# Kernel tuning notes

Measured on AMD Instinct MI355X. Metric: run time of the kernel, lower is better.

## Reference

```python
import jax, jax.numpy as jnp
import numpy as np

GRID_SIZE = 5
SPLINE_ORDER = 3
GRID_RANGE = (-0.2, 0.2)
N_TOK, IN_CH, OUT_CH = 8192, 1024, 1024
K_COEF = GRID_SIZE + SPLINE_ORDER  # 8 basis functions per feature


def _make_grid():
    lo, hi = GRID_RANGE
    h = (hi - lo) / GRID_SIZE
    # 12 knots, extended by spline_order on both sides
    return (jnp.arange(-SPLINE_ORDER, GRID_SIZE + SPLINE_ORDER + 1, dtype=jnp.float32) * h + lo)


def _b_splines(x, grid):
    # x: [N, in] -> bases: [N, in, K_COEF] via Cox-de Boor recursion
    xe = x[..., None]                      # [N, in, 1]
    G = grid.shape[0]                      # 12
    bases = ((xe >= grid[:-1]) & (xe < grid[1:])).astype(x.dtype)  # [N, in, G-1]
    for k in range(1, SPLINE_ORDER + 1):
        left = (xe - grid[: G - k - 1]) / (grid[k : G - 1] - grid[: G - k - 1]) * bases[..., :-1]
        right = (grid[k + 1 :] - xe) / (grid[k + 1 :] - grid[1 : G - k]) * bases[..., 1:]
        bases = left + right
    return bases                            # [N, in, 8]


def _kan_layer(x, base_w, spline_w, grid):
    # base_activation = Identity
    base_out = x @ base_w.T                               # [N, out]
    bases = _b_splines(x, grid)                           # [N, in, K]
    spline_out = jnp.einsum('nik,oik->no', bases, spline_w)
    return base_out + spline_out


def setup_inputs() -> dict:
    key = jax.random.key(0)
    k1, k2, k3, k4, k5 = jax.random.split(key, 5)
    lo, hi = GRID_RANGE
    x = jax.random.uniform(k1, (N_TOK, IN_CH), dtype=jnp.float32, minval=lo, maxval=hi)
    s = 0.1 / np.sqrt(IN_CH)
    return {
        'x': x,
        'base_w1': jax.random.normal(k2, (OUT_CH, IN_CH), dtype=jnp.float32) * s,
        'spline_w1': jax.random.normal(k3, (OUT_CH, IN_CH, K_COEF), dtype=jnp.float32) * s,
        'base_w2': jax.random.normal(k4, (OUT_CH, OUT_CH), dtype=jnp.float32) * s,
        'spline_w2': jax.random.normal(k5, (OUT_CH, OUT_CH, K_COEF), dtype=jnp.float32) * s,
    }


def reference(x, base_w1, spline_w1, base_w2, spline_w2):
    grid = _make_grid()
    x1 = _kan_layer(x, base_w1, spline_w1, grid)
    x2 = _kan_layer(x1, base_w2, spline_w2, grid)
    return x2
```

## Files before the change

kernel.cpp:

```cpp
#include <hip/hip_runtime.h>
#include <hip/hip_bf16.h>

typedef __attribute__((ext_vector_type(8))) short bf16x8;
typedef __attribute__((ext_vector_type(4))) float f32x4;

#define KCAT 9216
#define NTOK 8192
#define CH   1024
#define KHALF 4608
#define BK   64
#define NT   (KHALF / BK)

__device__ __forceinline__ unsigned short f2bf(float f) {
    union { float f; unsigned int u; } v; v.f = f;
    unsigned int r = v.u + 0x7fffu + ((v.u >> 16) & 1u);
    return (unsigned short)(r >> 16);
}

__device__ __forceinline__ void load16_to_lds(const void* gp, void* lp) {
    __builtin_amdgcn_global_load_lds(
        (__attribute__((address_space(1))) void*)(void*)gp,
        (__attribute__((address_space(3))) void*)lp,
        16, 0, 0);
}

__device__ __forceinline__ void bases8(float x, unsigned short* out8) {
    const float h = 0.08f;
    float t[12];
#pragma unroll
    for (int j = 0; j < 12; ++j) t[j] = -0.2f + h * (float)(j - 3);
    const float r1 = 1.0f / h, r2 = 1.0f / (2.0f * h), r3 = 1.0f / (3.0f * h);
    float b[11];
#pragma unroll
    for (int j = 0; j < 11; ++j) b[j] = (x >= t[j] && x < t[j + 1]) ? 1.0f : 0.0f;
#pragma unroll
    for (int j = 0; j < 10; ++j) b[j] = (x - t[j]) * r1 * b[j] + (t[j + 2] - x) * r1 * b[j + 1];
#pragma unroll
    for (int j = 0; j < 9; ++j)  b[j] = (x - t[j]) * r2 * b[j] + (t[j + 3] - x) * r2 * b[j + 1];
#pragma unroll
    for (int j = 0; j < 8; ++j)  b[j] = (x - t[j]) * r3 * b[j] + (t[j + 4] - x) * r3 * b[j + 1];
#pragma unroll
    for (int j = 0; j < 8; ++j) out8[j] = f2bf(b[j]);
}

__global__ __launch_bounds__(256) void conv_w(const float* __restrict__ BW,
                                              const float* __restrict__ SW,
                                              unsigned short* __restrict__ W) {
    int o = blockIdx.x;
    const float* bw = BW + (size_t)o * 1024;
    const float* sw = SW + (size_t)o * 8192;
    unsigned short* w = W + (size_t)o * KCAT;
    for (int c = threadIdx.x * 4; c < KCAT; c += 256 * 4) {
        const float* src = (c < 1024) ? (bw + c) : (sw + (c - 1024));
        float4 v = *(const float4*)src;
        unsigned short u[4] = { f2bf(v.x), f2bf(v.y), f2bf(v.z), f2bf(v.w) };
        *(unsigned long long*)(w + c) = *(unsigned long long*)u;
    }
}

__global__ __launch_bounds__(256) void kan_basis_x(const float* __restrict__ X,
                                                   unsigned short* __restrict__ A,
                                                   int total) {
    for (int idx = blockIdx.x * 256 + threadIdx.x; idx < total; idx += gridDim.x * 256) {
        int n = idx >> 10, i = idx & 1023;
        float x = X[idx];
        size_t rowbase = (size_t)n * KCAT;
        A[rowbase + i] = f2bf(x);
        unsigned short out8[8];
        bases8(x, out8);
        *(bf16x8*)(A + rowbase + 1024 + (size_t)i * 8) = *(bf16x8*)out8;
    }
}

__global__ __launch_bounds__(256) void kan_basis_sum(const float* __restrict__ C0,
                                                     const float* __restrict__ C1,
                                                     unsigned short* __restrict__ A,
                                                     int total) {
    for (int idx = blockIdx.x * 256 + threadIdx.x; idx < total; idx += gridDim.x * 256) {
        int n = idx >> 10, i = idx & 1023;
        float x = C0[idx] + C1[idx];
        size_t rowbase = (size_t)n * KCAT;
        A[rowbase + i] = f2bf(x);
        unsigned short out8[8];
        bases8(x, out8);
        *(bf16x8*)(A + rowbase + 1024 + (size_t)i * 8) = *(bf16x8*)out8;
    }
}

__global__ __launch_bounds__(256) void add_out(const float* __restrict__ C0,
                                               const float* __restrict__ C1,
                                               float* __restrict__ out, int total4) {
    for (int i = blockIdx.x * 256 + threadIdx.x; i < total4; i += gridDim.x * 256) {
        float4 a = ((const float4*)C0)[i];
        float4 b = ((const float4*)C1)[i];
        float4 r = { a.x + b.x, a.y + b.y, a.z + b.z, a.w + b.w };
        ((float4*)out)[i] = r;
    }
}

__global__ __launch_bounds__(512, 2) void gemm256_splitk(const unsigned short* __restrict__ A,
                                                         const unsigned short* __restrict__ B,
                                                         float* __restrict__ C0,
                                                         float* __restrict__ C1) {
    __shared__ unsigned short As[2 * 256 * 64];
    __shared__ unsigned short Bs[2 * 256 * 64];
    const int tid  = threadIdx.x;
    const int lane = tid & 63;
    const int wid  = tid >> 6;
    const int wr = wid >> 2, wc = wid & 3;
    const int ln = lane & 15, q = lane >> 4;

    const int bid = blockIdx.x;
    const int xcd = bid & 7, i = bid >> 3;
    const int kz = xcd & 1, chm = xcd >> 1;
    const int bm = chm * 8 + (i & 7);
    const int bn = i >> 3;

    const unsigned short* Ab = A + (size_t)(bm * 256) * KCAT + (size_t)kz * KHALF;
    const unsigned short* Bb = B + (size_t)(bn * 256) * KCAT + (size_t)kz * KHALF;
    float* C = (kz == 0) ? C0 : C1;

    f32x4 acc[8][4] = {};

    auto stage = [&](int t, int buf, int part) {
        int chunk = part * 512 + tid;
        int r    = chunk >> 3;
        int slot = (chunk & 7) ^ (r & 7);
        size_t goff = (size_t)r * (KCAT * 2) + (size_t)t * (BK * 2) + slot * 16;
        load16_to_lds((const char*)Ab + goff, (char*)As + (size_t)buf * 32768 + chunk * 16);
        load16_to_lds((const char*)Bb + goff, (char*)Bs + (size_t)buf * 32768 + chunk * 16);
    };

    stage(0, 0, 0); stage(0, 0, 1); stage(0, 0, 2); stage(0, 0, 3);
    asm volatile("s_waitcnt vmcnt(0)" ::: "memory");
    __builtin_amdgcn_s_barrier();

    for (int t = 0; t < NT; ++t) {
        const int c = t & 1;
        const char* Ap = (const char*)As + c * 32768;
        const char* Bp = (const char*)Bs + c * 32768;
        bf16x8 bfr[4][2];
        const bool pref = (t + 1 < NT);
#pragma unroll
        for (int p = 0; p < 4; ++p) {
            bf16x8 afr[2][2];
#pragma unroll
            for (int m2 = 0; m2 < 2; ++m2)
#pragma unroll
                for (int kh = 0; kh < 2; ++kh) {
                    int row = wr * 128 + (p * 2 + m2) * 16 + ln;
                    int byte = row * 128 + ((kh * 64 + q * 16) ^ ((row & 7) * 16));
                    afr[m2][kh] = *(const bf16x8*)(Ap + byte);
                }
            if (p == 0) {
#pragma unroll
                for (int nf = 0; nf < 4; ++nf)
#pragma unroll
                    for (int kh = 0; kh < 2; ++kh) {
                        int row = wc * 64 + nf * 16 + ln;
                        int byte = row * 128 + ((kh * 64 + q * 16) ^ ((row & 7) * 16));
                        bfr[nf][kh] = *(const bf16x8*)(Bp + byte);
                    }
            }
            if (pref) {
                if (p == 0)      { stage(t + 1, c ^ 1, 0); stage(t + 1, c ^ 1, 1); }
                else if (p == 1) { stage(t + 1, c ^ 1, 2); }
                else if (p == 2) { stage(t + 1, c ^ 1, 3); }
            }
            __builtin_amdgcn_s_barrier();
            asm volatile("s_waitcnt lgkmcnt(0)" ::: "memory");
            __builtin_amdgcn_sched_barrier(0);
            __builtin_amdgcn_s_setprio(1);
#pragma unroll
            for (int m2 = 0; m2 < 2; ++m2)
#pragma unroll
                for (int nf = 0; nf < 4; ++nf)
#pragma unroll
                    for (int kh = 0; kh < 2; ++kh)
                        acc[p * 2 + m2][nf] = __builtin_amdgcn_mfma_f32_16x16x32_bf16(
                            afr[m2][kh], bfr[nf][kh], acc[p * 2 + m2][nf], 0, 0, 0);
            __builtin_amdgcn_s_setprio(0);
            if (p == 3)
                asm volatile("s_waitcnt vmcnt(0)" ::: "memory");
            __builtin_amdgcn_s_barrier();
        }
    }

#pragma unroll
    for (int mf = 0; mf < 8; ++mf)
#pragma unroll
        for (int nf = 0; nf < 4; ++nf)
#pragma unroll
            for (int r = 0; r < 4; ++r) {
                int row = bm * 256 + wr * 128 + mf * 16 + q * 4 + r;
                int col = bn * 256 + wc * 64 + nf * 16 + ln;
                C[(size_t)row * CH + col] = acc[mf][nf][r];
            }
}

extern "C" void kernel_launch(void* const* d_in, const int* in_sizes, int n_in,
                              void* d_out, int out_size, void* d_ws, size_t ws_size,
                              hipStream_t stream) {
    const float* x   = (const float*)d_in[0];
    const float* bw1 = (const float*)d_in[1];
    const float* sw1 = (const float*)d_in[2];
    const float* bw2 = (const float*)d_in[3];
    const float* sw2 = (const float*)d_in[4];
    float* out = (float*)d_out;

    char* ws = (char*)d_ws;
    unsigned short* Abuf = (unsigned short*)ws;
    unsigned short* Wbuf = (unsigned short*)(ws + 150994944);
    float* C0 = (float*)(ws + 150994944 + 18874368);
    float* C1 = (float*)(ws + 150994944 + 18874368 + 33554432);

    dim3 blk(256);
    dim3 gW(1024);
    dim3 gB(2048);
    dim3 gG(256);
    dim3 blkG(512);

    conv_w        <<<gW, blk, 0, stream>>>(bw1, sw1, Wbuf);
    kan_basis_x   <<<gB, blk, 0, stream>>>(x, Abuf, NTOK * CH);
    gemm256_splitk<<<gG, blkG, 0, stream>>>(Abuf, Wbuf, C0, C1);

    conv_w        <<<gW, blk, 0, stream>>>(bw2, sw2, Wbuf);
    kan_basis_sum <<<gB, blk, 0, stream>>>(C0, C1, Abuf, NTOK * CH);
    gemm256_splitk<<<gG, blkG, 0, stream>>>(Abuf, Wbuf, C0, C1);
    add_out       <<<dim3(1024), blk, 0, stream>>>(C0, C1, out, NTOK * CH / 4);
}
```

Measured before the change: 506.7 us.

## Fuse B-spline basis generation into GEMM A-tile staging via closed-form cubic

```diff
diff --git a/kernel.cpp b/kernel.cpp
--- a/kernel.cpp
+++ b/kernel.cpp
@@ -3,6 +3,7 @@
 
 typedef __attribute__((ext_vector_type(8))) short bf16x8;
 typedef __attribute__((ext_vector_type(4))) float f32x4;
+typedef __attribute__((ext_vector_type(4))) unsigned int u32x4;
 
 #define KCAT 9216
 #define NTOK 8192
@@ -24,23 +25,33 @@
         16, 0, 0);
 }
 
-__device__ __forceinline__ void bases8(float x, unsigned short* out8) {
-    const float h = 0.08f;
-    float t[12];
-#pragma unroll
-    for (int j = 0; j < 12; ++j) t[j] = -0.2f + h * (float)(j - 3);
-    const float r1 = 1.0f / h, r2 = 1.0f / (2.0f * h), r3 = 1.0f / (3.0f * h);
-    float b[11];
-#pragma unroll
-    for (int j = 0; j < 11; ++j) b[j] = (x >= t[j] && x < t[j + 1]) ? 1.0f : 0.0f;
-#pragma unroll
-    for (int j = 0; j < 10; ++j) b[j] = (x - t[j]) * r1 * b[j] + (t[j + 2] - x) * r1 * b[j + 1];
-#pragma unroll
-    for (int j = 0; j < 9; ++j)  b[j] = (x - t[j]) * r2 * b[j] + (t[j + 3] - x) * r2 * b[j + 1];
-#pragma unroll
-    for (int j = 0; j < 8; ++j)  b[j] = (x - t[j]) * r3 * b[j] + (t[j + 4] - x) * r3 * b[j + 1];
-#pragma unroll
-    for (int j = 0; j < 8; ++j) out8[j] = f2bf(b[j]);
+__device__ __forceinline__ void bases8_cf(float x, unsigned int* w) {
+    float p  = (x + 0.44f) * 12.5f;
+    float mf = floorf(p);
+    float u  = p - mf;
+    int   m  = (int)mf;
+    float v  = 1.0f - u;
+    float u2 = u * u, u3 = u2 * u;
+    float N0 = v * v * v * (1.0f / 6.0f);
+    float N1 = 0.5f * u3 - u2 + (2.0f / 3.0f);
+    float N3 = u3 * (1.0f / 6.0f);
+    float N2 = 1.0f - N0 - N1 - N3;
+    unsigned long long lo =
+          (unsigned long long)f2bf(N0)
+        | ((unsigned long long)f2bf(N1) << 16)
+        | ((unsigned long long)f2bf(N2) << 32)
+        | ((unsigned long long)f2bf(N3) << 48);
+    lo = (m >= 0 && m <= 10) ? lo : 0ull;
+    int sh  = (m - 3) * 16;
+    int sh1 = sh - 64;
+    unsigned long long d0 =
+        (sh  >= 0) ? ((sh  < 64) ? (lo << sh)    : 0ull)
+                   : ((-sh  < 64) ? (lo >> (-sh))  : 0ull);
+    unsigned long long d1 =
+        (sh1 >= 0) ? ((sh1 < 64) ? (lo << sh1)   : 0ull)
+                   : ((-sh1 < 64) ? (lo >> (-sh1)) : 0ull);
+    w[0] = (unsigned int)d0; w[1] = (unsigned int)(d0 >> 32);
+    w[2] = (unsigned int)d1; w[3] = (unsigned int)(d1 >> 32);
 }
 
 __global__ __launch_bounds__(256) void conv_w(const float* __restrict__ BW,
@@ -58,32 +69,26 @@
     }
 }
 
-__global__ __launch_bounds__(256) void kan_basis_x(const float* __restrict__ X,
-                                                   unsigned short* __restrict__ A,
-                                                   int total) {
-    for (int idx = blockIdx.x * 256 + threadIdx.x; idx < total; idx += gridDim.x * 256) {
-        int n = idx >> 10, i = idx & 1023;
-        float x = X[idx];
-        size_t rowbase = (size_t)n * KCAT;
-        A[rowbase + i] = f2bf(x);
-        unsigned short out8[8];
-        bases8(x, out8);
-        *(bf16x8*)(A + rowbase + 1024 + (size_t)i * 8) = *(bf16x8*)out8;
-    }
-}
-
-__global__ __launch_bounds__(256) void kan_basis_sum(const float* __restrict__ C0,
-                                                     const float* __restrict__ C1,
-                                                     unsigned short* __restrict__ A,
-                                                     int total) {
-    for (int idx = blockIdx.x * 256 + threadIdx.x; idx < total; idx += gridDim.x * 256) {
-        int n = idx >> 10, i = idx & 1023;
-        float x = C0[idx] + C1[idx];
-        size_t rowbase = (size_t)n * KCAT;
-        A[rowbase + i] = f2bf(x);
-        unsigned short out8[8];
-        bases8(x, out8);
-        *(bf16x8*)(A + rowbase + 1024 + (size_t)i * 8) = *(bf16x8*)out8;
+__global__ __launch_bounds__(256) void kan_x(const float* __restrict__ X,
+                                             unsigned short* __restrict__ O, int total8) {
+    for (int i = blockIdx.x * 256 + threadIdx.x; i < total8; i += gridDim.x * 256) {
+        float4 a = ((const float4*)X)[i * 2];
+        float4 b = ((const float4*)X)[i * 2 + 1];
+        unsigned short o[8] = { f2bf(a.x), f2bf(a.y), f2bf(a.z), f2bf(a.w),
+                                f2bf(b.x), f2bf(b.y), f2bf(b.z), f2bf(b.w) };
+        *(bf16x8*)(O + (size_t)i * 8) = *(bf16x8*)o;
+    }
+}
+
+__global__ __launch_bounds__(256) void kan_x_sum(const float* __restrict__ A,
+                                                 const float* __restrict__ B,
+                                                 unsigned short* __restrict__ O, int total8) {
+    for (int i = blockIdx.x * 256 + threadIdx.x; i < total8; i += gridDim.x * 256) {
+        float4 a0 = ((const float4*)A)[i * 2],     b0 = ((const float4*)B)[i * 2];
+        float4 a1 = ((const float4*)A)[i * 2 + 1], b1 = ((const float4*)B)[i * 2 + 1];
+        unsigned short o[8] = { f2bf(a0.x + b0.x), f2bf(a0.y + b0.y), f2bf(a0.z + b0.z), f2bf(a0.w + b0.w),
+                                f2bf(a1.x + b1.x), f2bf(a1.y + b1.y), f2bf(a1.z + b1.z), f2bf(a1.w + b1.w) };
+        *(bf16x8*)(O + (size_t)i * 8) = *(bf16x8*)o;
     }
 }
 
@@ -98,12 +103,15 @@
     }
 }
 
-__global__ __launch_bounds__(512, 2) void gemm256_splitk(const unsigned short* __restrict__ A,
-                                                         const unsigned short* __restrict__ B,
-                                                         float* __restrict__ C0,
-                                                         float* __restrict__ C1) {
-    __shared__ unsigned short As[2 * 256 * 64];
-    __shared__ unsigned short Bs[2 * 256 * 64];
+template<bool SUM>
+__global__ __launch_bounds__(512, 2) void gemm_fused(const float* __restrict__ XA,
+                                                     const float* __restrict__ XB,
+                                                     const unsigned short* __restrict__ Xb16,
+                                                     const unsigned short* __restrict__ W,
+                                                     float* __restrict__ C0,
+                                                     float* __restrict__ C1) {
+    __shared__ __align__(16) unsigned short As[2 * 256 * 64];
+    __shared__ __align__(16) unsigned short Bs[2 * 256 * 64];
     const int tid  = threadIdx.x;
     const int lane = tid & 63;
     const int wid  = tid >> 6;
@@ -111,36 +119,76 @@
     const int ln = lane & 15, q = lane >> 4;
 
     const int bid = blockIdx.x;
-    const int xcd = bid & 7, i = bid >> 3;
+    const int xcd = bid & 7, ii = bid >> 3;
     const int kz = xcd & 1, chm = xcd >> 1;
-    const int bm = chm * 8 + (i & 7);
-    const int bn = i >> 3;
-
-    const unsigned short* Ab = A + (size_t)(bm * 256) * KCAT + (size_t)kz * KHALF;
-    const unsigned short* Bb = B + (size_t)(bn * 256) * KCAT + (size_t)kz * KHALF;
+    const int bm = chm * 8 + (ii & 7);
+    const int bn = ii >> 3;
+
+    const int sr  = tid >> 1;
+    const int sf0 = (tid & 1) * 4;
+
+    const unsigned short* Bb = W    + (size_t)(bn * 256) * KCAT + (size_t)kz * KHALF;
+    const unsigned short* Xb = Xb16 + (size_t)(bm * 256) * CH;
+    const float* xa = XA + (size_t)(bm * 256 + sr) * CH + sf0;
+    const float* xb = XB + (size_t)(bm * 256 + sr) * CH + sf0;
     float* C = (kz == 0) ? C0 : C1;
 
     f32x4 acc[8][4] = {};
 
-    auto stage = [&](int t, int buf, int part) {
+    auto stage_B = [&](int t, int d, int part) {
         int chunk = part * 512 + tid;
-        int r    = chunk >> 3;
+        int r = chunk >> 3;
         int slot = (chunk & 7) ^ (r & 7);
         size_t goff = (size_t)r * (KCAT * 2) + (size_t)t * (BK * 2) + slot * 16;
-        load16_to_lds((const char*)Ab + goff, (char*)As + (size_t)buf * 32768 + chunk * 16);
-        load16_to_lds((const char*)Bb + goff, (char*)Bs + (size_t)buf * 32768 + chunk * 16);
-    };
-
-    stage(0, 0, 0); stage(0, 0, 1); stage(0, 0, 2); stage(0, 0, 3);
-    asm volatile("s_waitcnt vmcnt(0)" ::: "memory");
+        load16_to_lds((const char*)Bb + goff, (char*)Bs + (size_t)d * 32768 + chunk * 16);
+    };
+    auto stage_Ab = [&](int t, int d, int part) {
+        int chunk = part * 512 + tid;
+        int r = chunk >> 3;
+        int slot = (chunk & 7) ^ (r & 7);
+        size_t goff = (size_t)r * (CH * 2) + (size_t)t * (BK * 2) + slot * 16;
+        load16_to_lds((const char*)Xb + goff, (char*)As + (size_t)d * 32768 + chunk * 16);
+    };
+    auto load_x = [&](int t) -> float4 {
+        int io = (kz == 0) ? (t * 8 - 128) : (448 + t * 8);
+        float4 xv = *(const float4*)(xa + io);
+        if (SUM) {
+            float4 y = *(const float4*)(xb + io);
+            xv.x += y.x; xv.y += y.y; xv.z += y.z; xv.w += y.w;
+        }
+        return xv;
+    };
+    auto spline_cw = [&](float4 xv, int d) {
+        char* basep = (char*)As + (size_t)d * 32768 + sr * 128;
+#pragma unroll
+        for (int j = 0; j < 4; ++j) {
+            float xj = (j == 0) ? xv.x : (j == 1) ? xv.y : (j == 2) ? xv.z : xv.w;
+            unsigned int wv[4];
+            bases8_cf(xj, wv);
+            *(u32x4*)(basep + (((sf0 + j) ^ (sr & 7)) * 16)) = (u32x4){wv[0], wv[1], wv[2], wv[3]};
+        }
+    };
+
+    if (kz == 0) {
+#pragma unroll
+        for (int part = 0; part < 4; ++part) { stage_Ab(0, 0, part); stage_B(0, 0, part); }
+    } else {
+        float4 xv = load_x(0);
+        spline_cw(xv, 0);
+#pragma unroll
+        for (int part = 0; part < 4; ++part) stage_B(0, 0, part);
+    }
+    asm volatile("s_waitcnt vmcnt(0) lgkmcnt(0)" ::: "memory");
     __builtin_amdgcn_s_barrier();
 
     for (int t = 0; t < NT; ++t) {
         const int c = t & 1;
         const char* Ap = (const char*)As + c * 32768;
         const char* Bp = (const char*)Bs + c * 32768;
+        const bool pref = (t + 1 < NT);
+        const bool nspl = pref && (kz == 1 || (t + 1) >= 16);
+        float4 xva;
         bf16x8 bfr[4][2];
-        const bool pref = (t + 1 < NT);
 #pragma unroll
         for (int p = 0; p < 4; ++p) {
             bf16x8 afr[2][2];
@@ -163,9 +211,21 @@
                     }
             }
             if (pref) {
-                if (p == 0)      { stage(t + 1, c ^ 1, 0); stage(t + 1, c ^ 1, 1); }
-                else if (p == 1) { stage(t + 1, c ^ 1, 2); }
-                else if (p == 2) { stage(t + 1, c ^ 1, 3); }
+                if (nspl) {
+                    if (p == 0) {
+                        xva = load_x(t + 1);
+                        stage_B(t + 1, c ^ 1, 0); stage_B(t + 1, c ^ 1, 1);
+                    } else if (p == 1) {
+                        stage_B(t + 1, c ^ 1, 2); stage_B(t + 1, c ^ 1, 3);
+                    } else if (p == 2) {
+                        spline_cw(xva, c ^ 1);
+                    }
+                } else {
+                    if (p == 0) { stage_Ab(t + 1, c ^ 1, 0); stage_Ab(t + 1, c ^ 1, 1);
+                                  stage_B (t + 1, c ^ 1, 0); stage_B (t + 1, c ^ 1, 1); }
+                    else if (p == 1) { stage_Ab(t + 1, c ^ 1, 2); stage_Ab(t + 1, c ^ 1, 3);
+                                       stage_B (t + 1, c ^ 1, 2); stage_B (t + 1, c ^ 1, 3); }
+                }
             }
             __builtin_amdgcn_s_barrier();
             asm volatile("s_waitcnt lgkmcnt(0)" ::: "memory");
@@ -209,23 +269,22 @@
     float* out = (float*)d_out;
 
     char* ws = (char*)d_ws;
-    unsigned short* Abuf = (unsigned short*)ws;
-    unsigned short* Wbuf = (unsigned short*)(ws + 150994944);
-    float* C0 = (float*)(ws + 150994944 + 18874368);
-    float* C1 = (float*)(ws + 150994944 + 18874368 + 33554432);
+    unsigned short* Wbuf = (unsigned short*)ws;
+    float* C0 = (float*)(ws + 18874368);
+    float* C1 = (float*)(ws + 52428800);
+    float* D0 = (float*)(ws + 85983232);
+    float* D1 = (float*)(ws + 119537664);
+    unsigned short* Xb  = (unsigned short*)(ws + 153092096);
+    unsigned short* X1b = (unsigned short*)(ws + 169869312);
 
     dim3 blk(256);
-    dim3 gW(1024);
-    dim3 gB(2048);
-    dim3 gG(256);
-    dim3 blkG(512);
-
-    conv_w        <<<gW, blk, 0, stream>>>(bw1, sw1, Wbuf);
-    kan_basis_x   <<<gB, blk, 0, stream>>>(x, Abuf, NTOK * CH);
-    gemm256_splitk<<<gG, blkG, 0, stream>>>(Abuf, Wbuf, C0, C1);
-
-    conv_w        <<<gW, blk, 0, stream>>>(bw2, sw2, Wbuf);
-    kan_basis_sum <<<gB, blk, 0, stream>>>(C0, C1, Abuf, NTOK * CH);
-    gemm256_splitk<<<gG, blkG, 0, stream>>>(Abuf, Wbuf, C0, C1);
-    add_out       <<<dim3(1024), blk, 0, stream>>>(C0, C1, out, NTOK * CH / 4);
-}
+
+    conv_w           <<<dim3(1024), blk, 0, stream>>>(bw1, sw1, Wbuf);
+    kan_x            <<<dim3(2048), blk, 0, stream>>>(x, Xb, NTOK * CH / 8);
+    gemm_fused<false><<<dim3(256), dim3(512), 0, stream>>>(x, x, Xb, Wbuf, C0, C1);
+
+    conv_w           <<<dim3(1024), blk, 0, stream>>>(bw2, sw2, Wbuf);
+    kan_x_sum        <<<dim3(2048), blk, 0, stream>>>(C0, C1, X1b, NTOK * CH / 8);
+    gemm_fused<true> <<<dim3(256), dim3(512), 0, stream>>>(C0, C1, X1b, Wbuf, D0, D1);
+    add_out          <<<dim3(1024), blk, 0, stream>>>(D0, D1, out, NTOK * CH / 4);
+}
```

New measurement: 568.7 us. +12.2%, slower.
